# Optimization experiments

Measured on AMD Instinct MI355X. Metric: run time of the kernel, lower is better.

The kernel has to match this reference:

```python
import jax, jax.numpy as jnp
import numpy as np

VOLUME_SIZE = 48  # max_disp / down = 192 / 4


def setup_inputs() -> dict:
    key = jax.random.key(0)
    k1, k2 = jax.random.split(key)
    b, c, h, w = 8, 128, 128, 240
    left_feature = jax.random.normal(k1, (b, c, h, w), dtype=jnp.float32)
    right_feature = jax.random.normal(k2, (b, c, h, w), dtype=jnp.float32)
    return {"left_feature": left_feature, "right_feature": right_feature}


def reference(left_feature, right_feature):
    # cost_volume[:, i, :, x] = mean_c(L[:, :, :, x] * R[:, :, :, x-i]) for x >= i, else 0
    b, c, h, w = left_feature.shape
    col = jnp.arange(w)

    def per_disp(i):
        # shift right feature right by i; zero out wrapped-around columns (< i)
        r_shift = jnp.roll(right_feature, i, axis=-1)  # [b,c,h,w]
        prod_mean = jnp.mean(left_feature * r_shift, axis=1)  # [b,h,w]
        return jnp.where(col >= i, prod_mean, 0.0)

    cv = jax.vmap(per_disp)(jnp.arange(VOLUME_SIZE))  # [V,b,h,w]
    return jnp.transpose(cv, (1, 0, 2, 3))  # [b,V,h,w]
```

## Files before the change

kernel.cpp:

```cpp
#include <hip/hip_runtime.h>
#include <hip/hip_fp16.h>

#define CV_B 8
#define CV_C 128
#define CV_H 128
#define CV_W 240
#define CV_V 48
#define PLANE (CV_H * CV_W)

#define NCP 4
#define NSTAGE 16
#define GUARDF 12
#define LROW 60
#define RROW (GUARDF + LROW)

typedef unsigned int u32x4 __attribute__((ext_vector_type(4)));

static __device__ __forceinline__ __half2 bc_h2(unsigned v) {
    return __builtin_bit_cast(__half2, v);
}
static __device__ __forceinline__ unsigned bc_u(__half2 v) {
    return __builtin_bit_cast(unsigned, v);
}

__global__ __launch_bounds__(256, 4) void cost_volume_kernel(
        const float* __restrict__ Lf, const float* __restrict__ Rf,
        float* __restrict__ out)
{
    __shared__ u32x4 sL[2][NCP][LROW];
    __shared__ u32x4 sR[2][NCP][RROW];

    const int t  = threadIdx.x;
    const int y  = blockIdx.x;
    const int b  = blockIdx.y;
    const int wv = t >> 6;
    const int u  = t & 63;
    const bool act = (u < 60);
    const int x0 = 4 * u;

    const float* Lrow = Lf + (size_t)(b * CV_C) * PLANE + y * CV_W;
    const float* Rrow = Rf + (size_t)(b * CV_C) * PLANE + y * CV_W;

    const int side = wv >> 1;
    const int a0   = (wv & 1) * 2;
    const float* Srow = side ? Rrow : Lrow;

    for (int idx = t; idx < 2 * NCP * GUARDF; idx += 256) {
        const int bi = idx / (NCP * GUARDF);
        const int rm = idx % (NCP * GUARDF);
        u32x4 z; z.x = 0u; z.y = 0u; z.z = 0u; z.w = 0u;
        sR[bi][rm / GUARDF][rm % GUARDF] = z;
    }

    float4 f0[2], f1[2];

    if (act) {
#pragma unroll
        for (int q = 0; q < 2; ++q) {
            const float* p = Srow + (size_t)(2 * (a0 + q)) * PLANE + x0;
            f0[q] = *(const float4*)p;
            f1[q] = *(const float4*)(p + PLANE);
        }
#pragma unroll
        for (int q = 0; q < 2; ++q) {
            u32x4 w;
            w.x = bc_u(__floats2half2_rn(f0[q].x, f1[q].x));
            w.y = bc_u(__floats2half2_rn(f0[q].y, f1[q].y));
            w.z = bc_u(__floats2half2_rn(f0[q].z, f1[q].z));
            w.w = bc_u(__floats2half2_rn(f0[q].w, f1[q].w));
            if (side) sR[0][a0 + q][GUARDF + u] = w;
            else      sL[0][a0 + q][u]          = w;
        }
    }
    __syncthreads();

    __half2 acc[4][12];
#pragma unroll
    for (int xx = 0; xx < 4; ++xx)
#pragma unroll
        for (int r = 0; r < 12; ++r) acc[xx][r] = __floats2half2_rn(0.f, 0.f);

    const int rbase = GUARDF - 3 - 3 * wv + u;

    for (int s = 0; s < NSTAGE; ++s) {
        const int P = s & 1;
        const bool pf = (s + 1 < NSTAGE);

        if (pf && act) {
#pragma unroll
            for (int q = 0; q < 2; ++q) {
                const float* p = Srow + (size_t)(8 * (s + 1) + 2 * (a0 + q)) * PLANE + x0;
                f0[q] = *(const float4*)p;
                f1[q] = *(const float4*)(p + PLANE);
            }
        }

        if (act) {
            const u32x4 (*__restrict__ sLp)[LROW] = sL[P];
            const u32x4 (*__restrict__ sRp)[RROW] = sR[P];
#pragma unroll
            for (int cp = 0; cp < NCP; ++cp) {
                const u32x4 lvv = sLp[cp][u];
                u32x4 rv[4];
#pragma unroll
                for (int kk = 0; kk < 4; ++kk)
                    rv[kk] = sRp[cp][rbase + kk];

                __half2 lw[4];
                lw[0] = bc_h2(lvv.x); lw[1] = bc_h2(lvv.y);
                lw[2] = bc_h2(lvv.z); lw[3] = bc_h2(lvv.w);
                __half2 rw[16];
#pragma unroll
                for (int kk = 0; kk < 4; ++kk) {
                    rw[4 * kk + 0] = bc_h2(rv[kk].x);
                    rw[4 * kk + 1] = bc_h2(rv[kk].y);
                    rw[4 * kk + 2] = bc_h2(rv[kk].z);
                    rw[4 * kk + 3] = bc_h2(rv[kk].w);
                }
#pragma unroll
                for (int r = 0; r < 12; ++r) {
#pragma unroll
                    for (int xx = 0; xx < 4; ++xx) {
                        const int m = xx + 12 - r;
                        acc[xx][r] = __hfma2(lw[xx], rw[m], acc[xx][r]);
                    }
                }
            }
        }

        if (pf && act) {
#pragma unroll
            for (int q = 0; q < 2; ++q) {
                u32x4 w;
                w.x = bc_u(__floats2half2_rn(f0[q].x, f1[q].x));
                w.y = bc_u(__floats2half2_rn(f0[q].y, f1[q].y));
                w.z = bc_u(__floats2half2_rn(f0[q].z, f1[q].z));
                w.w = bc_u(__floats2half2_rn(f0[q].w, f1[q].w));
                if (side) sR[P ^ 1][a0 + q][GUARDF + u] = w;
                else      sL[P ^ 1][a0 + q][u]          = w;
            }
        }
        if (pf) __syncthreads();
    }

    if (act) {
#pragma unroll
        for (int r = 0; r < 12; ++r) {
            const int i = 12 * wv + r;
            float4 o;
            o.x = (__low2float(acc[0][r]) + __high2float(acc[0][r])) * (1.f / 128.f);
            o.y = (__low2float(acc[1][r]) + __high2float(acc[1][r])) * (1.f / 128.f);
            o.z = (__low2float(acc[2][r]) + __high2float(acc[2][r])) * (1.f / 128.f);
            o.w = (__low2float(acc[3][r]) + __high2float(acc[3][r])) * (1.f / 128.f);
            *(float4*)&out[(((size_t)b * CV_V + i) * CV_H + y) * CV_W + x0] = o;
        }
    }
}

extern "C" void kernel_launch(void* const* d_in, const int* in_sizes, int n_in,
                              void* d_out, int out_size, void* d_ws, size_t ws_size,
                              hipStream_t stream)
{
    const float* Lf = (const float*)d_in[0];
    const float* Rf = (const float*)d_in[1];
    float* o = (float*)d_out;
    dim3 grid(CV_H, CV_B);
    dim3 block(256);
    hipLaunchKernelGGL(cost_volume_kernel, grid, block, 0, stream, Lf, Rf, o);
}
```

Measured before the change: 278.3 us.

## Split disparity range across two blocks per row to raise parallelism

Each (row, batch) is now handled by two blocks, each computing half of every wave's 12 disparities. Accumulators per thread drop from 48 to 24 half2 and shared-memory R reads per channel-pair drop from 4 to 3 vectors, with the aim of more blocks in flight and lower register pressure. The cost is that every block loads and converts the full L and R rows, which doubles global reads of the inputs.

```diff
diff --git a/kernel.cpp b/kernel.cpp
--- a/kernel.cpp
+++ b/kernel.cpp
@@ -23,6 +23,39 @@
     return __builtin_bit_cast(unsigned, v);
 }
 
+template <int M0P>
+static __device__ __forceinline__ void compute_stage(
+        const u32x4 (*__restrict__ sLp)[LROW],
+        const u32x4 (*__restrict__ sRp)[RROW],
+        int u, int rb, __half2 acc[4][6])
+{
+#pragma unroll
+    for (int cp = 0; cp < NCP; ++cp) {
+        const u32x4 lvv = sLp[cp][u];
+        const u32x4 rv0 = sRp[cp][rb];
+        const u32x4 rv1 = sRp[cp][rb + 1];
+        const u32x4 rv2 = sRp[cp][rb + 2];
+
+        __half2 lw[4];
+        lw[0] = bc_h2(lvv.x); lw[1] = bc_h2(lvv.y);
+        lw[2] = bc_h2(lvv.z); lw[3] = bc_h2(lvv.w);
+        __half2 rw[12];
+        rw[0] = bc_h2(rv0.x); rw[1]  = bc_h2(rv0.y);
+        rw[2] = bc_h2(rv0.z); rw[3]  = bc_h2(rv0.w);
+        rw[4] = bc_h2(rv1.x); rw[5]  = bc_h2(rv1.y);
+        rw[6] = bc_h2(rv1.z); rw[7]  = bc_h2(rv1.w);
+        rw[8] = bc_h2(rv2.x); rw[9]  = bc_h2(rv2.y);
+        rw[10] = bc_h2(rv2.z); rw[11] = bc_h2(rv2.w);
+#pragma unroll
+        for (int r = 0; r < 6; ++r) {
+#pragma unroll
+            for (int xx = 0; xx < 4; ++xx) {
+                acc[xx][r] = __hfma2(lw[xx], rw[xx + M0P - r], acc[xx][r]);
+            }
+        }
+    }
+}
+
 __global__ __launch_bounds__(256, 4) void cost_volume_kernel(
         const float* __restrict__ Lf, const float* __restrict__ Rf,
         float* __restrict__ out)
@@ -30,11 +63,12 @@
     __shared__ u32x4 sL[2][NCP][LROW];
     __shared__ u32x4 sR[2][NCP][RROW];
 
-    const int t  = threadIdx.x;
-    const int y  = blockIdx.x;
-    const int b  = blockIdx.y;
-    const int wv = t >> 6;
-    const int u  = t & 63;
+    const int t    = threadIdx.x;
+    const int iblk = blockIdx.x & 1;
+    const int y    = blockIdx.x >> 1;
+    const int b    = blockIdx.y;
+    const int wv   = t >> 6;
+    const int u    = t & 63;
     const bool act = (u < 60);
     const int x0 = 4 * u;
 
@@ -74,13 +108,13 @@
     }
     __syncthreads();
 
-    __half2 acc[4][12];
+    __half2 acc[4][6];
 #pragma unroll
     for (int xx = 0; xx < 4; ++xx)
 #pragma unroll
-        for (int r = 0; r < 12; ++r) acc[xx][r] = __floats2half2_rn(0.f, 0.f);
+        for (int r = 0; r < 6; ++r) acc[xx][r] = __floats2half2_rn(0.f, 0.f);
 
-    const int rbase = GUARDF - 3 - 3 * wv + u;
+    const int rb = iblk ? (u + 9 - 3 * wv) : (u + 10 - 3 * wv);
 
     for (int s = 0; s < NSTAGE; ++s) {
         const int P = s & 1;
@@ -96,36 +130,8 @@
         }
 
         if (act) {
-            const u32x4 (*__restrict__ sLp)[LROW] = sL[P];
-            const u32x4 (*__restrict__ sRp)[RROW] = sR[P];
-#pragma unroll
-            for (int cp = 0; cp < NCP; ++cp) {
-                const u32x4 lvv = sLp[cp][u];
-                u32x4 rv[4];
-#pragma unroll
-                for (int kk = 0; kk < 4; ++kk)
-                    rv[kk] = sRp[cp][rbase + kk];
-
-                __half2 lw[4];
-                lw[0] = bc_h2(lvv.x); lw[1] = bc_h2(lvv.y);
-                lw[2] = bc_h2(lvv.z); lw[3] = bc_h2(lvv.w);
-                __half2 rw[16];
-#pragma unroll
-                for (int kk = 0; kk < 4; ++kk) {
-                    rw[4 * kk + 0] = bc_h2(rv[kk].x);
-                    rw[4 * kk + 1] = bc_h2(rv[kk].y);
-                    rw[4 * kk + 2] = bc_h2(rv[kk].z);
-                    rw[4 * kk + 3] = bc_h2(rv[kk].w);
-                }
-#pragma unroll
-                for (int r = 0; r < 12; ++r) {
-#pragma unroll
-                    for (int xx = 0; xx < 4; ++xx) {
-                        const int m = xx + 12 - r;
-                        acc[xx][r] = __hfma2(lw[xx], rw[m], acc[xx][r]);
-                    }
-                }
-            }
+            if (iblk) compute_stage<6>(sL[P], sR[P], u, rb, acc);
+            else      compute_stage<8>(sL[P], sR[P], u, rb, acc);
         }
 
         if (pf && act) {
@@ -145,8 +151,8 @@
 
     if (act) {
 #pragma unroll
-        for (int r = 0; r < 12; ++r) {
-            const int i = 12 * wv + r;
+        for (int r = 0; r < 6; ++r) {
+            const int i = 12 * wv + 6 * iblk + r;
             float4 o;
             o.x = (__low2float(acc[0][r]) + __high2float(acc[0][r])) * (1.f / 128.f);
             o.y = (__low2float(acc[1][r]) + __high2float(acc[1][r])) * (1.f / 128.f);
@@ -164,7 +170,7 @@
     const float* Lf = (const float*)d_in[0];
     const float* Rf = (const float*)d_in[1];
     float* o = (float*)d_out;
-    dim3 grid(CV_H, CV_B);
+    dim3 grid(2 * CV_H, CV_B);
     dim3 block(256);
     hipLaunchKernelGGL(cost_volume_kernel, grid, block, 0, stream, Lf, Rf, o);
 }
```

New measurement: 279.8 us. About the same (+0.5%).
